# Performance work log

Hardware: AMD Instinct MI355X
Metric: run time of the kernel (lower is better)

Reference implementation:

```python
import jax, jax.numpy as jnp
import numpy as np

N = 2048
D = 1024
H = 16
DK = D // H
TOPK = 128
LN_EPS = 1e-5


def setup_inputs() -> dict:
    key = jax.random.key(0)
    ks = jax.random.split(key, 16)
    s = 1.0 / np.sqrt(D)
    sh = 1.0 / np.sqrt(H)
    return {
        "x": jax.random.normal(ks[0], (N, D), jnp.float32),
        "Wq": jax.random.normal(ks[1], (D, D), jnp.float32) * s,
        "bq": jnp.zeros((D,), jnp.float32),
        "Wk": jax.random.normal(ks[2], (D, D), jnp.float32) * s,
        "bk": jnp.zeros((D,), jnp.float32),
        "Wv": jax.random.normal(ks[3], (D, D), jnp.float32) * s,
        "bv": jnp.zeros((D,), jnp.float32),
        "Wpre": jax.random.normal(ks[4], (H, H), jnp.float32) * sh,
        "bpre": jnp.zeros((H,), jnp.float32),
        "Wpost": jax.random.normal(ks[5], (H, H), jnp.float32) * sh,
        "bpost": jnp.zeros((H,), jnp.float32),
        "Wo": jax.random.normal(ks[6], (D, D), jnp.float32) * s,
        "bo": jnp.zeros((D,), jnp.float32),
        "gamma": jnp.ones((D,), jnp.float32),
        "beta": jnp.zeros((D,), jnp.float32),
    }


def _layernorm(x, gamma, beta):
    mu = jnp.mean(x, axis=-1, keepdims=True)
    var = jnp.var(x, axis=-1, keepdims=True)
    return (x - mu) * jax.lax.rsqrt(var + LN_EPS) * gamma + beta


def reference(x, Wq, bq, Wk, bk, Wv, bv, Wpre, bpre, Wpost, bpost, Wo, bo, gamma, beta):
    n, d = x.shape
    residual = x
    xn = _layernorm(x, gamma, beta)
    # projections -> (n, H, dk)
    q = (xn @ Wq.T + bq).reshape(n, H, DK)
    k = (xn @ Wk.T + bk).reshape(n, H, DK)
    v = (xn @ Wv.T + bv).reshape(n, H, DK)
    scale = 1.0 / np.sqrt(float(DK))
    # full scores (H, n, n); torch chunking over q is math-equivalent (dropout=0)
    scores = jnp.einsum('qhd,khd->hqk', q, k) * scale
    # pre-softmax talking heads: mix over head axis (nn.Linear on last dim h)
    scores = jnp.einsum('hqk,gh->gqk', scores, Wpre) + bpre[:, None, None]
    attn = jax.nn.softmax(scores, axis=-1)
    # top-k sparsify + renormalize (threshold mask == torch scatter mask for distinct values)
    kth = jax.lax.top_k(attn, TOPK)[0][..., -1:]
    attn = jnp.where(attn >= kth, attn, 0.0)
    attn = attn / (jnp.sum(attn, axis=-1, keepdims=True) + 1e-9)
    # post-softmax talking heads
    attn = jnp.einsum('hqk,gh->gqk', attn, Wpost) + bpost[:, None, None]
    out = jnp.einsum('hqk,khd->qhd', attn, v).reshape(n, d)
    return residual + out @ Wo.T + bo
```

## Files before the change

### kernel.cpp

```cpp
#include <hip/hip_runtime.h>
#include <stdint.h>

typedef unsigned short u16;
using bf16x8 = __attribute__((ext_vector_type(8))) short;
using f32x4  = __attribute__((ext_vector_type(4))) float;

#define N_TOK 2048
#define DMODEL 1024
#define NHEAD 16
#define HDK 64
#define TOPK_K 128

__device__ __forceinline__ u16 f2b(float f) {
  unsigned u = __float_as_uint(f);
  return (u16)((u + 0x7FFFu + ((u >> 16) & 1u)) >> 16);
}
__device__ __forceinline__ float b2f(u16 b) {
  return __uint_as_float(((unsigned)b) << 16);
}
__device__ __forceinline__ float wave_reduce_sum(float v) {
#pragma unroll
  for (int d = 32; d >= 1; d >>= 1) v += __shfl_xor(v, d);
  return v;
}
__device__ __forceinline__ unsigned bits2key(unsigned u) {
  return (u & 0x80000000u) ? ~u : (u | 0x80000000u);
}
__device__ __forceinline__ float key2f(unsigned k) {
  unsigned u = (k & 0x80000000u) ? (k ^ 0x80000000u) : ~k;
  return __uint_as_float(u);
}

__global__ __launch_bounds__(256) void ln_kernel(const float* __restrict__ x,
                                                 const float* __restrict__ gamma,
                                                 const float* __restrict__ beta,
                                                 u16* __restrict__ xn) {
  int w = threadIdx.x >> 6, lane = threadIdx.x & 63;
  int row = blockIdx.x * 4 + w;
  const float4* xr = (const float4*)(x + (size_t)row * DMODEL);
  float4 v[4];
  float s = 0.f, ss = 0.f;
#pragma unroll
  for (int i = 0; i < 4; ++i) {
    v[i] = xr[i * 64 + lane];
    s += v[i].x + v[i].y + v[i].z + v[i].w;
    ss += v[i].x * v[i].x + v[i].y * v[i].y + v[i].z * v[i].z + v[i].w * v[i].w;
  }
  s = wave_reduce_sum(s);
  ss = wave_reduce_sum(ss);
  float mu = s * (1.f / DMODEL);
  float var = ss * (1.f / DMODEL) - mu * mu;
  float rstd = rsqrtf(var + 1e-5f);
  const float4* g4 = (const float4*)gamma;
  const float4* b4 = (const float4*)beta;
  u16* xo = xn + (size_t)row * DMODEL;
#pragma unroll
  for (int i = 0; i < 4; ++i) {
    float4 g = g4[i * 64 + lane], b = b4[i * 64 + lane];
    float ox = (v[i].x - mu) * rstd * g.x + b.x;
    float oy = (v[i].y - mu) * rstd * g.y + b.y;
    float oz = (v[i].z - mu) * rstd * g.z + b.z;
    float ow = (v[i].w - mu) * rstd * g.w + b.w;
    unsigned lo = (unsigned)f2b(ox) | ((unsigned)f2b(oy) << 16);
    unsigned hi = (unsigned)f2b(oz) | ((unsigned)f2b(ow) << 16);
    *(uint2*)&xo[(i * 64 + lane) * 4] = make_uint2(lo, hi);
  }
}

__global__ __launch_bounds__(256) void cast_kernel(const float* __restrict__ in,
                                                   u16* __restrict__ out, int n8) {
  int i = blockIdx.x * 256 + threadIdx.x;
  if (i >= n8) return;
  const float4* p = (const float4*)in + (size_t)i * 2;
  float4 a = p[0], b = p[1];
  unsigned w0 = (unsigned)f2b(a.x) | ((unsigned)f2b(a.y) << 16);
  unsigned w1 = (unsigned)f2b(a.z) | ((unsigned)f2b(a.w) << 16);
  unsigned w2 = (unsigned)f2b(b.x) | ((unsigned)f2b(b.y) << 16);
  unsigned w3 = (unsigned)f2b(b.z) | ((unsigned)f2b(b.w) << 16);
  *(uint4*)&out[(size_t)i * 8] = make_uint4(w0, w1, w2, w3);
}

__global__ __launch_bounds__(256) void concat3_kernel(const float* __restrict__ a,
                                                      const float* __restrict__ b,
                                                      const float* __restrict__ c,
                                                      float* __restrict__ out) {
  int i = blockIdx.x * 256 + threadIdx.x;
  if (i < 1024) out[i] = a[i];
  else if (i < 2048) out[i] = b[i - 1024];
  else if (i < 3072) out[i] = c[i - 2048];
}

__global__ __launch_bounds__(256) void transpose_kernel(const u16* __restrict__ V, int ldv,
                                                        u16* __restrict__ Vt) {
  __shared__ u16 tile[64][72];
  int kb = blockIdx.x * 64, cb = blockIdx.y * 64;
  int t = threadIdx.x;
  int r = t >> 2, cg = (t & 3) * 16;
  *(uint4*)&tile[r][cg]     = *(const uint4*)&V[(size_t)(kb + r) * ldv + cb + cg];
  *(uint4*)&tile[r][cg + 8] = *(const uint4*)&V[(size_t)(kb + r) * ldv + cb + cg + 8];
  __syncthreads();
  int c = t >> 2, kg = (t & 3) * 16;
  size_t base = (size_t)(cb + c) * N_TOK + kb + kg;
  unsigned p0 = (unsigned)tile[kg + 0][c] | ((unsigned)tile[kg + 1][c] << 16);
  unsigned p1 = (unsigned)tile[kg + 2][c] | ((unsigned)tile[kg + 3][c] << 16);
  unsigned p2 = (unsigned)tile[kg + 4][c] | ((unsigned)tile[kg + 5][c] << 16);
  unsigned p3 = (unsigned)tile[kg + 6][c] | ((unsigned)tile[kg + 7][c] << 16);
  unsigned p4 = (unsigned)tile[kg + 8][c] | ((unsigned)tile[kg + 9][c] << 16);
  unsigned p5 = (unsigned)tile[kg + 10][c] | ((unsigned)tile[kg + 11][c] << 16);
  unsigned p6 = (unsigned)tile[kg + 12][c] | ((unsigned)tile[kg + 13][c] << 16);
  unsigned p7 = (unsigned)tile[kg + 14][c] | ((unsigned)tile[kg + 15][c] << 16);
  *(uint4*)&Vt[base]     = make_uint4(p0, p1, p2, p3);
  *(uint4*)&Vt[base + 8] = make_uint4(p4, p5, p6, p7);
}

__global__ __launch_bounds__(256) void gemm_bf16_nt(
    const u16* __restrict__ A, int lda, int az,
    const u16* __restrict__ B, int ldb, int bz,
    void* __restrict__ Cv, int ldc, int cz,
    int K, float scale,
    const float* __restrict__ bias,
    const float* __restrict__ res, int out_f32) {
  __shared__ u16 As[64 * 40];
  __shared__ u16 Bs[64 * 40];
  A += (size_t)blockIdx.z * az;
  B += (size_t)blockIdx.z * bz;
  int bi = blockIdx.y * 64, bj = blockIdx.x * 64;
  int tid = threadIdx.x;
  int w = tid >> 6, lane = tid & 63;
  int wr = w >> 1, wc = w & 1;
  int lr = tid >> 2, lc = (tid & 3) * 8;
  int kh = (lane >> 4) * 8, fr = lane & 15;
  f32x4 acc[2][2] = {};
  for (int k0 = 0; k0 < K; k0 += 32) {
    *(uint4*)&As[lr * 40 + lc] = *(const uint4*)&A[(size_t)(bi + lr) * lda + k0 + lc];
    *(uint4*)&Bs[lr * 40 + lc] = *(const uint4*)&B[(size_t)(bj + lr) * ldb + k0 + lc];
    __syncthreads();
    bf16x8 a0 = *(bf16x8*)&As[(wr * 32 + fr) * 40 + kh];
    bf16x8 a1 = *(bf16x8*)&As[(wr * 32 + 16 + fr) * 40 + kh];
    bf16x8 b0 = *(bf16x8*)&Bs[(wc * 32 + fr) * 40 + kh];
    bf16x8 b1 = *(bf16x8*)&Bs[(wc * 32 + 16 + fr) * 40 + kh];
    acc[0][0] = __builtin_amdgcn_mfma_f32_16x16x32_bf16(a0, b0, acc[0][0], 0, 0, 0);
    acc[0][1] = __builtin_amdgcn_mfma_f32_16x16x32_bf16(a0, b1, acc[0][1], 0, 0, 0);
    acc[1][0] = __builtin_amdgcn_mfma_f32_16x16x32_bf16(a1, b0, acc[1][0], 0, 0, 0);
    acc[1][1] = __builtin_amdgcn_mfma_f32_16x16x32_bf16(a1, b1, acc[1][1], 0, 0, 0);
    __syncthreads();
  }
  float* Cf = (float*)Cv + (size_t)blockIdx.z * cz;
  u16* Ch = (u16*)Cv + (size_t)blockIdx.z * cz;
  int rg = (lane >> 4) * 4;
#pragma unroll
  for (int m = 0; m < 2; ++m) {
#pragma unroll
    for (int n = 0; n < 2; ++n) {
      int gcol = bj + wc * 32 + n * 16 + fr;
      float badd = bias ? bias[gcol] : 0.f;
#pragma unroll
      for (int r = 0; r < 4; ++r) {
        int grow = bi + wr * 32 + m * 16 + rg + r;
        size_t off = (size_t)grow * ldc + gcol;
        float v = acc[m][n][r] * scale + badd;
        if (res) v += res[off];
        if (out_f32) Cf[off] = v;
        else Ch[off] = f2b(v);
      }
    }
  }
}

__global__ __launch_bounds__(256) void headmix_kernel(
    const u16* __restrict__ in, const float* __restrict__ W,
    const float* __restrict__ bias, void* __restrict__ out, int out_f32) {
  __shared__ u16 tile[NHEAD][512];
  __shared__ float w_s[256];
  __shared__ float b_s[16];
  int q = blockIdx.x, kb = blockIdx.y * 512;
  int t = threadIdx.x;
  w_s[t] = W[t];
  if (t < 16) b_s[t] = bias ? bias[t] : 0.f;
#pragma unroll
  for (int j = 0; j < 4; ++j) {
    int idx = j * 256 + t;
    int h = idx >> 6, cu = idx & 63;
    ((uint4*)&tile[h][0])[cu] =
        ((const uint4*)(in + ((size_t)q * NHEAD + h) * N_TOK + kb))[cu];
  }
  __syncthreads();
  float sv0[16], sv1[16];
#pragma unroll
  for (int h = 0; h < 16; ++h) {
    unsigned pw = ((const unsigned*)&tile[h][0])[t];
    sv0[h] = b2f((u16)(pw & 0xFFFFu));
    sv1[h] = b2f((u16)(pw >> 16));
  }
#pragma unroll
  for (int g = 0; g < 16; ++g) {
    float a0 = b_s[g], a1 = b_s[g];
#pragma unroll
    for (int h = 0; h < 16; ++h) {
      float wv = w_s[g * 16 + h];
      a0 = fmaf(wv, sv0[h], a0);
      a1 = fmaf(wv, sv1[h], a1);
    }
    size_t obase = ((size_t)q * NHEAD + g) * N_TOK + kb;
    if (out_f32) {
      ((float2*)((float*)out + obase))[t] = make_float2(a0, a1);
    } else {
      ((unsigned*)((u16*)out + obase))[t] =
          (unsigned)f2b(a0) | ((unsigned)f2b(a1) << 16);
    }
  }
}

__global__ __launch_bounds__(256, 4) void topk_rows_kernel(
    const float* __restrict__ S2, u16* __restrict__ S) {
  int row = blockIdx.x * 4 + (threadIdx.x >> 6);
  int lane = threadIdx.x & 63;
  const uint4* rp = (const uint4*)(S2 + (size_t)row * N_TOK);
  unsigned key[32];
#pragma unroll
  for (int i = 0; i < 8; ++i) {
    uint4 u = rp[i * 64 + lane];
    key[i * 4 + 0] = bits2key(u.x);
    key[i * 4 + 1] = bits2key(u.y);
    key[i * 4 + 2] = bits2key(u.z);
    key[i * 4 + 3] = bits2key(u.w);
  }
  unsigned kmax = 0u;
#pragma unroll
  for (int j = 0; j < 32; ++j) kmax = key[j] > kmax ? key[j] : kmax;
#pragma unroll
  for (int d = 32; d >= 1; d >>= 1) {
    unsigned o = (unsigned)__shfl_xor((int)kmax, d);
    kmax = o > kmax ? o : kmax;
  }
  float mx = key2f(kmax);
  unsigned T = 0u;
#pragma unroll 1
  for (int bit = 31; bit >= 0; --bit) {
    unsigned cand = T | (1u << bit);
    int c = 0;
#pragma unroll
    for (int j = 0; j < 32; ++j)
      c += (int)__popcll(__ballot(key[j] >= cand));
    if (c >= TOPK_K) T = cand;
  }
  float e[32];
  float z = 0.f, ms = 0.f;
#pragma unroll
  for (int j = 0; j < 32; ++j) {
    float ev = __expf(key2f(key[j]) - mx);
    e[j] = ev;
    z += ev;
    if (key[j] >= T) ms += ev;
  }
  z = wave_reduce_sum(z);
  ms = wave_reduce_sum(ms);
  float cs = 1.f / (ms + 1e-9f * z);
  u16* op = S + (size_t)row * N_TOK;
#pragma unroll
  for (int i = 0; i < 8; ++i) {
    unsigned pk[4];
#pragma unroll
    for (int c2 = 0; c2 < 4; ++c2) {
      unsigned k = key[i * 4 + c2];
      float val = (k >= T) ? e[i * 4 + c2] * cs : 0.f;
      pk[c2] = (unsigned)f2b(val);
    }
    uint2 w2;
    w2.x = pk[0] | (pk[1] << 16);
    w2.y = pk[2] | (pk[3] << 16);
    ((uint2*)op)[i * 64 + lane] = w2;
  }
}

extern "C" void kernel_launch(void* const* d_in, const int* in_sizes, int n_in,
                              void* d_out, int out_size, void* d_ws, size_t ws_size,
                              hipStream_t stream) {
  const float* x     = (const float*)d_in[0];
  const float* Wq    = (const float*)d_in[1];
  const float* bq    = (const float*)d_in[2];
  const float* Wk    = (const float*)d_in[3];
  const float* bk    = (const float*)d_in[4];
  const float* Wv    = (const float*)d_in[5];
  const float* bv    = (const float*)d_in[6];
  const float* Wpre  = (const float*)d_in[7];
  const float* Wpost = (const float*)d_in[9];
  const float* bpost = (const float*)d_in[10];
  const float* Wo    = (const float*)d_in[11];
  const float* bo    = (const float*)d_in[12];
  const float* gamma = (const float*)d_in[13];
  const float* beta  = (const float*)d_in[14];

  const size_t NM = (size_t)N_TOK * DMODEL;
  const size_t WW = (size_t)DMODEL * DMODEL;
  const int D3 = 3 * DMODEL;
  char* p = (char*)d_ws;
  u16* xnb   = (u16*)p; p += NM * 2;
  u16* QKVb  = (u16*)p; p += (size_t)N_TOK * D3 * 2;
  u16* Vtb   = (u16*)p; p += NM * 2;
  u16* AOb   = (u16*)p; p += NM * 2;
  u16* WQKVb = (u16*)p; p += 3 * WW * 2;
  u16* Wob   = (u16*)p; p += WW * 2;
  float* bqkv = (float*)p; p += D3 * 4;
  size_t base = (size_t)(p - (char*)d_ws);

  int CQ = 0;
  const int cands[6] = {2048, 1024, 512, 256, 128, 64};
  for (int i = 0; i < 6; ++i) {
    size_t need = base + (size_t)cands[i] * NHEAD * N_TOK * (2 + 4);
    if (need <= ws_size) { CQ = cands[i]; break; }
  }
  if (CQ == 0) return;
  u16* S    = (u16*)p;
  float* S2 = (float*)(p + (size_t)CQ * NHEAD * N_TOK * 2);

  ln_kernel<<<N_TOK / 4, 256, 0, stream>>>(x, gamma, beta, xnb);
  cast_kernel<<<512, 256, 0, stream>>>(Wq, WQKVb, WW / 8);
  cast_kernel<<<512, 256, 0, stream>>>(Wk, WQKVb + WW, WW / 8);
  cast_kernel<<<512, 256, 0, stream>>>(Wv, WQKVb + 2 * WW, WW / 8);
  cast_kernel<<<512, 256, 0, stream>>>(Wo, Wob, WW / 8);
  concat3_kernel<<<12, 256, 0, stream>>>(bq, bk, bv, bqkv);

  gemm_bf16_nt<<<dim3(48, 32, 1), 256, 0, stream>>>(xnb, DMODEL, 0, WQKVb, DMODEL, 0,
                                                    QKVb, D3, 0, DMODEL, 1.f, bqkv, nullptr, 0);
  transpose_kernel<<<dim3(N_TOK / 64, DMODEL / 64), 256, 0, stream>>>(QKVb + 2048, D3, Vtb);

  for (int q0 = 0; q0 < N_TOK; q0 += CQ) {
    gemm_bf16_nt<<<dim3(N_TOK / 64, CQ / 64, NHEAD), 256, 0, stream>>>(
        QKVb + (size_t)q0 * D3, D3, HDK, QKVb + 1024, D3, HDK,
        S, NHEAD * N_TOK, N_TOK, HDK, 0.125f, nullptr, nullptr, 0);

    headmix_kernel<<<dim3(CQ, 4), 256, 0, stream>>>(S, Wpre, nullptr, S2, 1);

    topk_rows_kernel<<<CQ * NHEAD / 4, 256, 0, stream>>>(S2, S);

    headmix_kernel<<<dim3(CQ, 4), 256, 0, stream>>>(S, Wpost, bpost, S, 0);

    gemm_bf16_nt<<<dim3(1, CQ / 64, NHEAD), 256, 0, stream>>>(
        S, NHEAD * N_TOK, N_TOK, Vtb, N_TOK, HDK * N_TOK,
        AOb + (size_t)q0 * DMODEL, DMODEL, HDK, N_TOK, 1.f, nullptr, nullptr, 0);
  }

  gemm_bf16_nt<<<dim3(16, 32, 1), 256, 0, stream>>>(AOb, DMODEL, 0, Wob, DMODEL, 0,
                                                    d_out, DMODEL, 0, DMODEL, 1.f, bo, x, 1);
}
```

Measured before the change: 568.9 us.

## Fuse pre-softmax head mixing into top-k kernel and drop fp32 score buffer

Replaces the separate pre-mix headmix kernel, which wrote fp32 mixed scores, and the top-k kernel with one kernel. The fused kernel reads the 16 bf16 head rows per query, mixes them in registers, then runs the radix top-k and softmax renormalisation. This removes a full fp32 write and read of the score tensor, and the smaller workspace need can allow a larger query chunk. It also adds an early exit from the bit search when the count equals k, and recomputes the exponentials at write time instead of keeping them in registers. Each block now reads all 16 heads for its query, so the same input rows are read again by the four blocks per query.

Result: faster. 486.8 us (-14.4%).

```diff
diff --git a/kernel.cpp b/kernel.cpp
--- a/kernel.cpp
+++ b/kernel.cpp
@@ -211,23 +211,55 @@
   }
 }
 
-__global__ __launch_bounds__(256, 4) void topk_rows_kernel(
-    const float* __restrict__ S2, u16* __restrict__ S) {
-  int row = blockIdx.x * 4 + (threadIdx.x >> 6);
+#define ACCS_APPLY(OP) \
+  OP(0, A0.x, A0.y)  OP(1, A0.z, A0.w)  OP(2, A1.x, A1.y)  OP(3, A1.z, A1.w) \
+  OP(4, A2.x, A2.y)  OP(5, A2.z, A2.w)  OP(6, A3.x, A3.y)  OP(7, A3.z, A3.w) \
+  OP(8, A4.x, A4.y)  OP(9, A4.z, A4.w)  OP(10, A5.x, A5.y) OP(11, A5.z, A5.w) \
+  OP(12, A6.x, A6.y) OP(13, A6.z, A6.w) OP(14, A7.x, A7.y) OP(15, A7.z, A7.w)
+#define KEYS_APPLY(OP) \
+  OP(Q0.x) OP(Q0.y) OP(Q0.z) OP(Q0.w) OP(Q1.x) OP(Q1.y) OP(Q1.z) OP(Q1.w) \
+  OP(Q2.x) OP(Q2.y) OP(Q2.z) OP(Q2.w) OP(Q3.x) OP(Q3.y) OP(Q3.z) OP(Q3.w) \
+  OP(Q4.x) OP(Q4.y) OP(Q4.z) OP(Q4.w) OP(Q5.x) OP(Q5.y) OP(Q5.z) OP(Q5.w) \
+  OP(Q6.x) OP(Q6.y) OP(Q6.z) OP(Q6.w) OP(Q7.x) OP(Q7.y) OP(Q7.z) OP(Q7.w)
+
+__global__ __launch_bounds__(256, 4) void premix_topk_kernel(
+    const u16* __restrict__ Sin, const float* __restrict__ Wpre,
+    u16* __restrict__ Sout) {
+  int bid = blockIdx.x;
+  int q = bid >> 2;
+  int g = ((bid & 3) << 2) + (threadIdx.x >> 6);
   int lane = threadIdx.x & 63;
-  const uint4* rp = (const uint4*)(S2 + (size_t)row * N_TOK);
-  unsigned key[32];
-#pragma unroll
-  for (int i = 0; i < 8; ++i) {
-    uint4 u = rp[i * 64 + lane];
-    key[i * 4 + 0] = bits2key(u.x);
-    key[i * 4 + 1] = bits2key(u.y);
-    key[i * 4 + 2] = bits2key(u.z);
-    key[i * 4 + 3] = bits2key(u.w);
+  const u16* slab = Sin + (size_t)q * (NHEAD * N_TOK);
+
+  float4 A0 = {0,0,0,0}, A1 = {0,0,0,0}, A2 = {0,0,0,0}, A3 = {0,0,0,0};
+  float4 A4 = {0,0,0,0}, A5 = {0,0,0,0}, A6 = {0,0,0,0}, A7 = {0,0,0,0};
+#pragma unroll
+  for (int h = 0; h < 16; ++h) {
+    float wv = Wpre[g * 16 + h];
+    const u16* rowp = slab + (size_t)h * N_TOK + 2 * lane;
+#define PM(m, LO, HI) { unsigned pw = *(const unsigned*)(rowp + 128 * (m)); \
+      LO = fmaf(wv, b2f((u16)(pw & 0xFFFFu)), LO); \
+      HI = fmaf(wv, b2f((u16)(pw >> 16)), HI); }
+    ACCS_APPLY(PM)
+#undef PM
+  }
+  uint4 Q0, Q1, Q2, Q3, Q4, Q5, Q6, Q7;
+  {
+#define NK_IDX(F, AF) F = bits2key(__float_as_uint(AF));
+    NK_IDX(Q0.x, A0.x) NK_IDX(Q0.y, A0.y) NK_IDX(Q0.z, A0.z) NK_IDX(Q0.w, A0.w)
+    NK_IDX(Q1.x, A1.x) NK_IDX(Q1.y, A1.y) NK_IDX(Q1.z, A1.z) NK_IDX(Q1.w, A1.w)
+    NK_IDX(Q2.x, A2.x) NK_IDX(Q2.y, A2.y) NK_IDX(Q2.z, A2.z) NK_IDX(Q2.w, A2.w)
+    NK_IDX(Q3.x, A3.x) NK_IDX(Q3.y, A3.y) NK_IDX(Q3.z, A3.z) NK_IDX(Q3.w, A3.w)
+    NK_IDX(Q4.x, A4.x) NK_IDX(Q4.y, A4.y) NK_IDX(Q4.z, A4.z) NK_IDX(Q4.w, A4.w)
+    NK_IDX(Q5.x, A5.x) NK_IDX(Q5.y, A5.y) NK_IDX(Q5.z, A5.z) NK_IDX(Q5.w, A5.w)
+    NK_IDX(Q6.x, A6.x) NK_IDX(Q6.y, A6.y) NK_IDX(Q6.z, A6.z) NK_IDX(Q6.w, A6.w)
+    NK_IDX(Q7.x, A7.x) NK_IDX(Q7.y, A7.y) NK_IDX(Q7.z, A7.z) NK_IDX(Q7.w, A7.w)
+#undef NK_IDX
   }
   unsigned kmax = 0u;
-#pragma unroll
-  for (int j = 0; j < 32; ++j) kmax = key[j] > kmax ? key[j] : kmax;
+#define MX(KF) kmax = (KF) > kmax ? (KF) : kmax;
+  KEYS_APPLY(MX)
+#undef MX
 #pragma unroll
   for (int d = 32; d >= 1; d >>= 1) {
     unsigned o = (unsigned)__shfl_xor((int)kmax, d);
@@ -239,38 +271,29 @@
   for (int bit = 31; bit >= 0; --bit) {
     unsigned cand = T | (1u << bit);
     int c = 0;
-#pragma unroll
-    for (int j = 0; j < 32; ++j)
-      c += (int)__popcll(__ballot(key[j] >= cand));
+#define CNT(KF) c += (int)__popcll(__ballot((KF) >= cand));
+    KEYS_APPLY(CNT)
+#undef CNT
     if (c >= TOPK_K) T = cand;
-  }
-  float e[32];
+    if (c == TOPK_K) break;
+  }
   float z = 0.f, ms = 0.f;
-#pragma unroll
-  for (int j = 0; j < 32; ++j) {
-    float ev = __expf(key2f(key[j]) - mx);
-    e[j] = ev;
-    z += ev;
-    if (key[j] >= T) ms += ev;
-  }
+#define ES(KF) { float ev = __expf(key2f(KF) - mx); z += ev; if ((KF) >= T) ms += ev; }
+  KEYS_APPLY(ES)
+#undef ES
   z = wave_reduce_sum(z);
   ms = wave_reduce_sum(ms);
   float cs = 1.f / (ms + 1e-9f * z);
-  u16* op = S + (size_t)row * N_TOK;
-#pragma unroll
-  for (int i = 0; i < 8; ++i) {
-    unsigned pk[4];
-#pragma unroll
-    for (int c2 = 0; c2 < 4; ++c2) {
-      unsigned k = key[i * 4 + c2];
-      float val = (k >= T) ? e[i * 4 + c2] * cs : 0.f;
-      pk[c2] = (unsigned)f2b(val);
-    }
-    uint2 w2;
-    w2.x = pk[0] | (pk[1] << 16);
-    w2.y = pk[2] | (pk[3] << 16);
-    ((uint2*)op)[i * 64 + lane] = w2;
-  }
+  u16* op = Sout + ((size_t)q * NHEAD + g) * N_TOK + 2 * lane;
+#define WB(m, LO, HI) { \
+    float e0 = (LO >= T) ? __expf(key2f(LO) - mx) * cs : 0.f; \
+    float e1 = (HI >= T) ? __expf(key2f(HI) - mx) * cs : 0.f; \
+    *(unsigned*)(op + 128 * (m)) = (unsigned)f2b(e0) | ((unsigned)f2b(e1) << 16); }
+  {
+    uint4 A0 = Q0, A1 = Q1, A2 = Q2, A3 = Q3, A4 = Q4, A5 = Q5, A6 = Q6, A7 = Q7;
+    ACCS_APPLY(WB)
+  }
+#undef WB
 }
 
 extern "C" void kernel_launch(void* const* d_in, const int* in_sizes, int n_in,
@@ -307,12 +330,12 @@
   int CQ = 0;
   const int cands[6] = {2048, 1024, 512, 256, 128, 64};
   for (int i = 0; i < 6; ++i) {
-    size_t need = base + (size_t)cands[i] * NHEAD * N_TOK * (2 + 4);
+    size_t need = base + (size_t)cands[i] * NHEAD * N_TOK * 4;
     if (need <= ws_size) { CQ = cands[i]; break; }
   }
   if (CQ == 0) return;
-  u16* S    = (u16*)p;
-  float* S2 = (float*)(p + (size_t)CQ * NHEAD * N_TOK * 2);
+  u16* Sa = (u16*)p;
+  u16* Sb = (u16*)(p + (size_t)CQ * NHEAD * N_TOK * 2);
 
   ln_kernel<<<N_TOK / 4, 256, 0, stream>>>(x, gamma, beta, xnb);
   cast_kernel<<<512, 256, 0, stream>>>(Wq, WQKVb, WW / 8);
@@ -328,16 +351,14 @@
   for (int q0 = 0; q0 < N_TOK; q0 += CQ) {
     gemm_bf16_nt<<<dim3(N_TOK / 64, CQ / 64, NHEAD), 256, 0, stream>>>(
         QKVb + (size_t)q0 * D3, D3, HDK, QKVb + 1024, D3, HDK,
-        S, NHEAD * N_TOK, N_TOK, HDK, 0.125f, nullptr, nullptr, 0);
-
-    headmix_kernel<<<dim3(CQ, 4), 256, 0, stream>>>(S, Wpre, nullptr, S2, 1);
-
-    topk_rows_kernel<<<CQ * NHEAD / 4, 256, 0, stream>>>(S2, S);
-
-    headmix_kernel<<<dim3(CQ, 4), 256, 0, stream>>>(S, Wpost, bpost, S, 0);
+        Sa, NHEAD * N_TOK, N_TOK, HDK, 0.125f, nullptr, nullptr, 0);
+
+    premix_topk_kernel<<<CQ * 4, 256, 0, stream>>>(Sa, Wpre, Sb);
+
+    headmix_kernel<<<dim3(CQ, 4), 256, 0, stream>>>(Sb, Wpost, bpost, Sb, 0);
 
     gemm_bf16_nt<<<dim3(1, CQ / 64, NHEAD), 256, 0, stream>>>(
-        S, NHEAD * N_TOK, N_TOK, Vtb, N_TOK, HDK * N_TOK,
+        Sb, NHEAD * N_TOK, N_TOK, Vtb, N_TOK, HDK * N_TOK,
         AOb + (size_t)q0 * DMODEL, DMODEL, HDK, N_TOK, 1.f, nullptr, nullptr, 0);
   }
 
```
